# Kernel optimization log

Measured on AMD Instinct MI355X. Metric: run time of the kernel, lower is better.

## Reference

```python
import jax, jax.numpy as jnp
import numpy as np

N = 50000      # nodes
E = 800000     # edges (avg degree 16)
DIM = 256      # in_channels == heads * out_channels
H = 8          # heads
C = DIM // H   # per-head out_channels = 32
EDGE_DIM = 2
NEG_SLOPE = 0.2


def setup_inputs() -> dict:
    key = jax.random.key(0)
    ks = jax.random.split(key, 8)
    x = jax.random.normal(ks[0], (N, DIM), dtype=jnp.float32)
    edge_index = jax.random.randint(ks[1], (2, E), 0, N, dtype=jnp.int32)
    edge_attr = jax.random.normal(ks[2], (E, EDGE_DIM), dtype=jnp.float32)
    s = 1.0 / np.sqrt(DIM)
    W_l = jax.random.normal(ks[3], (DIM, H * C), dtype=jnp.float32) * s   # lin_l (src)
    W_r = jax.random.normal(ks[4], (DIM, H * C), dtype=jnp.float32) * s   # lin_r (dst)
    W_e = jax.random.normal(ks[5], (EDGE_DIM, H * C), dtype=jnp.float32) * (1.0 / np.sqrt(EDGE_DIM))
    att = jax.random.normal(ks[6], (H, C), dtype=jnp.float32) * s         # attention vector a
    bias = jnp.zeros((H * C,), dtype=jnp.float32)
    return {"x": x, "edge_index": edge_index, "edge_attr": edge_attr,
            "W_l": W_l, "W_r": W_r, "W_e": W_e, "att": att, "bias": bias}


def reference(x, edge_index, edge_attr, W_l, W_r, W_e, att, bias):
    src, dst = edge_index[0], edge_index[1]
    # --- add self loops; fill_value='mean' => scatter-mean of incoming edge_attr per node ---
    attr_sum = jax.ops.segment_sum(edge_attr, dst, num_segments=N)          # [N, 2]
    cnt = jax.ops.segment_sum(jnp.ones((edge_attr.shape[0], 1), edge_attr.dtype), dst, num_segments=N)
    loop_attr = attr_sum / jnp.maximum(cnt, 1.0)                             # [N, 2], 0 for isolated nodes
    idx = jnp.arange(N, dtype=src.dtype)
    src_a = jnp.concatenate([src, idx])                                      # [E+N]
    dst_a = jnp.concatenate([dst, idx])
    ea = jnp.concatenate([edge_attr, loop_attr], axis=0)                     # [E+N, 2]
    # --- GATv2: project src/dst/edge features ---
    x_l = (x @ W_l).reshape(N, H, C)
    x_r = (x @ W_r).reshape(N, H, C)
    e_e = (ea @ W_e).reshape(-1, H, C)                                       # [E+N, H, C]
    m = x_l[src_a] + x_r[dst_a] + e_e                                        # [E+N, H, C]
    score = jnp.einsum('ehc,hc->eh', jax.nn.leaky_relu(m, NEG_SLOPE), att)   # [E+N, H]
    # --- segment softmax over incoming edges of each dst (self loop guarantees >=1 edge) ---
    smax = jax.ops.segment_max(score, dst_a, num_segments=N)                 # [N, H]
    ex = jnp.exp(score - smax[dst_a])
    denom = jax.ops.segment_sum(ex, dst_a, num_segments=N)                   # [N, H]
    alpha = ex / denom[dst_a]                                                # [E+N, H]
    # --- weighted scatter-add of src messages ---
    out = jax.ops.segment_sum(alpha[..., None] * x_l[src_a], dst_a, num_segments=N)  # [N, H, C]
    return out.reshape(N, H * C) + bias
```

## Files before the change

### kernel.cpp

```cpp
#include <hip/hip_runtime.h>
#include <hip/hip_bf16.h>

#define NN 50000
#define EE 800000
#define DIM 256
#define ROWC 64
#define NEG_SLOPE 0.2f
#define LOG2E 1.44269504088896f

#define GEMM_BLOCKS 1564
#define CF_BLOCKS   3125
#define ZERO_BLOCKS 49
#define WT_BLOCKS   512

typedef __attribute__((ext_vector_type(8))) short short8;
typedef __attribute__((ext_vector_type(4))) float f32x4;
typedef __attribute__((ext_vector_type(2))) float v2f;

__device__ __forceinline__ unsigned short f2bf(float f) {
    unsigned u = __float_as_uint(f);
    unsigned r = (u + 0x7fffu + ((u >> 16) & 1u)) >> 16;
    return (unsigned short)r;
}
__device__ __forceinline__ float u2f_lo(unsigned u) {
    return __uint_as_float(u << 16);
}
__device__ __forceinline__ float u2f_hi(unsigned u) {
    return __uint_as_float(u & 0xffff0000u);
}

__device__ __forceinline__ float red8(float s) {
    int t;
    t = __builtin_amdgcn_update_dpp(0, __float_as_int(s), 0xB1, 0xF, 0xF, true);
    s += __int_as_float(t);
    t = __builtin_amdgcn_update_dpp(0, __float_as_int(s), 0x4E, 0xF, 0xF, true);
    s += __int_as_float(t);
    t = __builtin_amdgcn_update_dpp(0, __float_as_int(s), 0x141, 0xF, 0xF, true);
    s += __int_as_float(t);
    return s;
}

__global__ __launch_bounds__(256) void k_prep0(
    const float* __restrict__ Wl, const float* __restrict__ Wr,
    unsigned short* __restrict__ wt, int* __restrict__ cnt)
{
    int b = blockIdx.x;
    if (b < ZERO_BLOCKS) {
        *(int4*)(cnt + (b * 256 + threadIdx.x) * 4) = make_int4(0, 0, 0, 0);
    } else {
        int idx = (b - ZERO_BLOCKS) * 256 + threadIdx.x;
        int n = idx >> 8, k = idx & 255;
        float v = (n < 256) ? Wl[k * 256 + n] : Wr[k * 256 + (n - 256)];
        wt[idx] = f2bf(v);
    }
}

__global__ __launch_bounds__(256) void k_main(
    const float* __restrict__ x, const unsigned short* __restrict__ wt,
    const int* __restrict__ ei, const float* __restrict__ ea,
    int* __restrict__ cnt, unsigned short* __restrict__ xl,
    unsigned short* __restrict__ xr, uint2* __restrict__ edge_rec)
{
    __shared__ short sAB[12288];
    int tid = threadIdx.x;

    if (blockIdx.x >= GEMM_BLOCKS) {
        int e = (blockIdx.x - GEMM_BLOCKS) * 256 + tid;
        int src = ei[e];
        int dst = ei[EE + e];
        float2 a = *(const float2*)(ea + 2 * e);
        int rl = atomicAdd(cnt + dst, 1);
        if (rl < ROWC) {
            unsigned packed = ((unsigned)f2bf(a.y) << 16) | f2bf(a.x);
            edge_rec[(size_t)dst * ROWC + rl] = make_uint2((unsigned)src, packed);
        }
        return;
    }

    int bid = blockIdx.x;
    const int q = GEMM_BLOCKS / 8, r = GEMM_BLOCKS % 8;
    int xcd = bid & 7, kk = bid >> 3;
    int wg = (xcd < r) ? xcd * (q + 1) + kk
                       : r * (q + 1) + (xcd - r) * q + kk;

    int wid = tid >> 6, lane = tid & 63;
    int mt = wg >> 2, nt = wg & 3;
    int mBase = mt * 128, nBase = nt * 128;
    int wm = (wid & 1) * 64, wn = (wid >> 1) * 64;
    int qq4 = lane >> 4, mh = lane & 15;

    f32x4 acc[4][4];
#pragma unroll
    for (int i = 0; i < 4; ++i)
#pragma unroll
        for (int j = 0; j < 4; ++j)
            acc[i][j] = (f32x4){0.f, 0.f, 0.f, 0.f};

    int aoffF[4], boff[4];
#pragma unroll
    for (int f = 0; f < 4; ++f) {
        int rr = wm + f * 16 + mh;
        aoffF[f] = rr * 32 + ((qq4 ^ (rr & 3)) << 3);
        int nl = wn + f * 16 + mh;
        boff[f] = 8192 + (nl * 4 + (qq4 ^ (nl & 3))) * 8;
    }

    for (int k0 = 0; k0 < 256; k0 += 32) {
        __syncthreads();
#pragma unroll
        for (int it = 0; it < 6; ++it) {
            int L = it * 256 + tid;
            const void* g;
            if (L < 1024) {
                int rr = L >> 3;
                int qs = (L >> 1) & 3, hf = L & 1;
                int q2 = qs ^ (rr & 3);
                int grow = mBase + rr;
                if (grow > NN - 1) grow = NN - 1;
                g = (const void*)(x + (size_t)grow * 256 + k0 + q2 * 8 + hf * 4);
            } else {
                int LB = L - 1024;
                int nl = LB >> 2;
                int q2 = (LB & 3) ^ (nl & 3);
                g = (const void*)(wt + (size_t)(nBase + nl) * 256 + k0 + q2 * 8);
            }
            short* lp = sAB + (it * 256 + wid * 64) * 8;
            __builtin_amdgcn_global_load_lds(
                (const __attribute__((address_space(1))) void*)g,
                (__attribute__((address_space(3))) void*)lp, 16, 0, 0);
        }
        __syncthreads();

        short8 af[4], bfr[4];
        const float* sAf = (const float*)sAB;
#pragma unroll
        for (int f = 0; f < 4; ++f) {
            f32x4 lo = *(const f32x4*)(sAf + aoffF[f]);
            f32x4 hi = *(const f32x4*)(sAf + aoffF[f] + 4);
            uint4 up;
            asm("v_cvt_pk_bf16_f32 %0, %1, %2" : "=v"(up.x) : "v"(lo[0]), "v"(lo[1]));
            asm("v_cvt_pk_bf16_f32 %0, %1, %2" : "=v"(up.y) : "v"(lo[2]), "v"(lo[3]));
            asm("v_cvt_pk_bf16_f32 %0, %1, %2" : "=v"(up.z) : "v"(hi[0]), "v"(hi[1]));
            asm("v_cvt_pk_bf16_f32 %0, %1, %2" : "=v"(up.w) : "v"(hi[2]), "v"(hi[3]));
            af[f] = *(short8*)&up;
        }
#pragma unroll
        for (int f = 0; f < 4; ++f) bfr[f] = *(const short8*)(sAB + boff[f]);
#pragma unroll
        for (int i = 0; i < 4; ++i)
#pragma unroll
            for (int j = 0; j < 4; ++j)
                acc[i][j] = __builtin_amdgcn_mfma_f32_16x16x32_bf16(
                    af[i], bfr[j], acc[i][j], 0, 0, 0);
    }

    unsigned short* cb = (nt < 2) ? xl : xr;
    int chalf = (nt & 1) * 128;
#pragma unroll
    for (int i = 0; i < 4; ++i)
#pragma unroll
        for (int j = 0; j < 4; ++j)
#pragma unroll
            for (int rr = 0; rr < 4; ++rr) {
                int row = mBase + wm + i * 16 + qq4 * 4 + rr;
                if (row < NN) {
                    int col = chalf + wn + j * 16 + mh;
                    cb[(size_t)row * 256 + col] = f2bf(acc[i][j][rr]);
                }
            }
}

__global__ __launch_bounds__(256) void k_attn(
    const unsigned short* __restrict__ xl, const unsigned short* __restrict__ xr,
    const int* __restrict__ cnt, const uint2* __restrict__ edge_rec,
    const float* __restrict__ W_e, const float* __restrict__ att,
    const float* __restrict__ bias, float* __restrict__ out)
{
    int n = __builtin_amdgcn_readfirstlane(blockIdx.x * 4 + (threadIdx.x >> 6));
    if (n >= NN) return;
    int lane = threadIdx.x & 63;
    int j = lane * 4;

    uint2 xru = *(const uint2*)(xr + ((size_t)n << 8) + j);
    v2f xr01 = {u2f_lo(xru.x), u2f_hi(xru.x)};
    v2f xr23 = {u2f_lo(xru.y), u2f_hi(xru.y)};
    float4 av = *(const float4*)(att + j);
    v2f att01 = {av.x * LOG2E, av.y * LOG2E};
    v2f att23 = {av.z * LOG2E, av.w * LOG2E};
    float4 w0v = *(const float4*)(W_e + j);
    float4 w1v = *(const float4*)(W_e + 256 + j);
    v2f we0_01 = {w0v.x, w0v.y}, we0_23 = {w0v.z, w0v.w};
    v2f we1_01 = {w1v.x, w1v.y}, we1_23 = {w1v.z, w1v.w};
    const v2f sl2 = {NEG_SLOPE, NEG_SLOPE};

    int cn = __builtin_amdgcn_readfirstlane(cnt[n]);
    if (cn > ROWC) cn = ROWC;
    int rs = n << 6;

    float D = 0.0f, la0 = 0.0f, la1 = 0.0f;
    v2f acc01 = {0.f, 0.f}, acc23 = {0.f, 0.f};

    auto body = [&](uint2 ru, float a0, float a1) {
        v2f xl01 = {u2f_lo(ru.x), u2f_hi(ru.x)};
        v2f xl23 = {u2f_lo(ru.y), u2f_hi(ru.y)};
        v2f a0v = {a0, a0}, a1v = {a1, a1};
        v2f m01 = xl01 + xr01;
        v2f m23 = xl23 + xr23;
        m01 = __builtin_elementwise_fma(a0v, we0_01, m01);
        m23 = __builtin_elementwise_fma(a0v, we0_23, m23);
        m01 = __builtin_elementwise_fma(a1v, we1_01, m01);
        m23 = __builtin_elementwise_fma(a1v, we1_23, m23);
        v2f t01 = __builtin_elementwise_max(m01, m01 * sl2);
        v2f t23 = __builtin_elementwise_max(m23, m23 * sl2);
        v2f sv = t01 * att01;
        sv = __builtin_elementwise_fma(t23, att23, sv);
        float s = sv.x + sv.y;
        s = red8(s);
        float w = __builtin_amdgcn_exp2f(s);
        D += w;
        v2f wv = {w, w};
        acc01 = __builtin_elementwise_fma(wv, xl01, acc01);
        acc23 = __builtin_elementwise_fma(wv, xl23, acc23);
    };

    if (cn > 0) {
        uint2 rc = edge_rec[rs + lane];
        int rcx = (int)rc.x, rca = (int)rc.y;

        auto gat = [&](int k) -> uint2 {
            unsigned sidx = (unsigned)__builtin_amdgcn_readlane(rcx, k);
            if (sidx > NN - 1) sidx = 0;
            return *(const uint2*)(xl + ((size_t)sidx << 8) + j);
        };
        auto proc = [&](uint2 xu, int k) {
            unsigned pk = (unsigned)__builtin_amdgcn_readlane(rca, k);
            float a0 = __uint_as_float(pk << 16);
            float a1 = __uint_as_float(pk & 0xffff0000u);
            la0 += a0; la1 += a1;
            body(xu, a0, a1);
        };

        int m = cn;
        uint2 x0 = gat(0), x1 = gat(1), x2 = gat(2), x3 = gat(3);
        uint2 x4 = gat(4), x5 = gat(5), x6 = gat(6), x7 = gat(7);
        for (int i = 0; i < m; i += 8) {
            proc(x0, i);
            if (i +  8 < m) x0 = gat(i +  8);
            if (i + 1 < m) { proc(x1, i + 1); if (i +  9 < m) x1 = gat(i +  9); }
            if (i + 2 < m) { proc(x2, i + 2); if (i + 10 < m) x2 = gat(i + 10); }
            if (i + 3 < m) { proc(x3, i + 3); if (i + 11 < m) x3 = gat(i + 11); }
            if (i + 4 < m) { proc(x4, i + 4); if (i + 12 < m) x4 = gat(i + 12); }
            if (i + 5 < m) { proc(x5, i + 5); if (i + 13 < m) x5 = gat(i + 13); }
            if (i + 6 < m) { proc(x6, i + 6); if (i + 14 < m) x6 = gat(i + 14); }
            if (i + 7 < m) { proc(x7, i + 7); if (i + 15 < m) x7 = gat(i + 15); }
        }
    }

    float invc = 1.0f / fmaxf((float)cn, 1.0f);
    uint2 xs = *(const uint2*)(xl + ((size_t)n << 8) + j);
    body(xs, la0 * invc, la1 * invc);

    float invD = 1.0f / D;
    float4 b4 = *(const float4*)(bias + j);
    float4 o;
    o.x = fmaf(acc01.x, invD, b4.x);
    o.y = fmaf(acc01.y, invD, b4.y);
    o.z = fmaf(acc23.x, invD, b4.z);
    o.w = fmaf(acc23.y, invD, b4.w);
    *(float4*)(out + (size_t)n * 256 + j) = o;
}

extern "C" void kernel_launch(void* const* d_in, const int* in_sizes, int n_in,
                              void* d_out, int out_size, void* d_ws, size_t ws_size,
                              hipStream_t stream)
{
    const float* x    = (const float*)d_in[0];
    const int*   ei   = (const int*)  d_in[1];
    const float* ea   = (const float*)d_in[2];
    const float* Wl   = (const float*)d_in[3];
    const float* Wr   = (const float*)d_in[4];
    const float* We   = (const float*)d_in[5];
    const float* att  = (const float*)d_in[6];
    const float* bias = (const float*)d_in[7];
    float* out = (float*)d_out;

    char* ws = (char*)d_ws;
    size_t off = 0;
    unsigned short* xl = (unsigned short*)(ws + off); off += (size_t)NN * 256 * 2;
    unsigned short* xr = (unsigned short*)(ws + off); off += (size_t)NN * 256 * 2;
    uint2*  edge_rec   = (uint2*)(ws + off);          off += (size_t)(NN * ROWC + 128) * 8;
    int*    cnt        = (int*)(ws + off);            off += (size_t)(ZERO_BLOCKS * 1024) * 4;
    unsigned short* wt = (unsigned short*)(ws + off); off += (size_t)512 * 256 * 2;

    k_prep0 <<<ZERO_BLOCKS + WT_BLOCKS, 256, 0, stream>>>(Wl, Wr, wt, cnt);
    k_main  <<<GEMM_BLOCKS + CF_BLOCKS, 256, 0, stream>>>(
        x, wt, ei, ea, cnt, xl, xr, edge_rec);
    k_attn  <<<12500, 256, 0, stream>>>(
        xl, xr, cnt, edge_rec, We, att, bias, out);
}
```

Measured before the change: 242.8 us.

## Split edge bucketing by destination range and overlap with attention kernels

Edge bucketing is split into three destination-node ranges. The first runs alongside the GEMM and the next two run inside the attention launches for node ranges already fully bucketed. The attention work is split across three kernels so each range's scatter overlaps with compute on earlier ranges. In exchange, the destination indices are re-read three times and an extra kernel launch is added.

```diff
diff --git a/kernel.cpp b/kernel.cpp
--- a/kernel.cpp
+++ b/kernel.cpp
@@ -8,10 +8,16 @@
 #define NEG_SLOPE 0.2f
 #define LOG2E 1.44269504088896f
 
+#define D1 16668
+#define D2 33336
+
+#define CF_BLOCKS   3125
 #define GEMM_BLOCKS 1564
-#define CF_BLOCKS   3125
 #define ZERO_BLOCKS 49
 #define WT_BLOCKS   512
+#define ATTN_A_BLOCKS 4167
+#define ATTN_B_BLOCKS 4167
+#define ATTN_C_BLOCKS 4166
 
 typedef __attribute__((ext_vector_type(8))) short short8;
 typedef __attribute__((ext_vector_type(4))) float f32x4;
@@ -40,6 +46,122 @@
     return s;
 }
 
+__device__ __forceinline__ void cf_range(
+    const int* __restrict__ ei, const float* __restrict__ ea,
+    int* __restrict__ cnt, uint2* __restrict__ edge_rec,
+    int blk, int tid, int dlo, int dhi)
+{
+    int e = blk * 256 + tid;
+    int dst = ei[EE + e];
+    if (dst >= dlo && dst < dhi) {
+        int src = ei[e];
+        float2 a = *(const float2*)(ea + 2 * e);
+        int rl = atomicAdd(cnt + dst, 1);
+        if (rl < ROWC) {
+            unsigned packed = ((unsigned)f2bf(a.y) << 16) | f2bf(a.x);
+            edge_rec[(size_t)dst * ROWC + rl] = make_uint2((unsigned)src, packed);
+        }
+    }
+}
+
+__device__ __forceinline__ void attn_node(
+    const unsigned short* __restrict__ xl, const unsigned short* __restrict__ xr,
+    const int* __restrict__ cnt, const uint2* __restrict__ edge_rec,
+    const float* __restrict__ W_e, const float* __restrict__ att,
+    const float* __restrict__ bias, float* __restrict__ out,
+    int n, int lane)
+{
+    int j = lane * 4;
+
+    uint2 xru = *(const uint2*)(xr + ((size_t)n << 8) + j);
+    v2f xr01 = {u2f_lo(xru.x), u2f_hi(xru.x)};
+    v2f xr23 = {u2f_lo(xru.y), u2f_hi(xru.y)};
+    float4 av = *(const float4*)(att + j);
+    v2f att01 = {av.x * LOG2E, av.y * LOG2E};
+    v2f att23 = {av.z * LOG2E, av.w * LOG2E};
+    float4 w0v = *(const float4*)(W_e + j);
+    float4 w1v = *(const float4*)(W_e + 256 + j);
+    v2f we0_01 = {w0v.x, w0v.y}, we0_23 = {w0v.z, w0v.w};
+    v2f we1_01 = {w1v.x, w1v.y}, we1_23 = {w1v.z, w1v.w};
+    const v2f sl2 = {NEG_SLOPE, NEG_SLOPE};
+
+    int cn = __builtin_amdgcn_readfirstlane(cnt[n]);
+    if (cn > ROWC) cn = ROWC;
+    int rs = n << 6;
+
+    float D = 0.0f, la0 = 0.0f, la1 = 0.0f;
+    v2f acc01 = {0.f, 0.f}, acc23 = {0.f, 0.f};
+
+    auto body = [&](uint2 ru, float a0, float a1) {
+        v2f xl01 = {u2f_lo(ru.x), u2f_hi(ru.x)};
+        v2f xl23 = {u2f_lo(ru.y), u2f_hi(ru.y)};
+        v2f a0v = {a0, a0}, a1v = {a1, a1};
+        v2f m01 = xl01 + xr01;
+        v2f m23 = xl23 + xr23;
+        m01 = __builtin_elementwise_fma(a0v, we0_01, m01);
+        m23 = __builtin_elementwise_fma(a0v, we0_23, m23);
+        m01 = __builtin_elementwise_fma(a1v, we1_01, m01);
+        m23 = __builtin_elementwise_fma(a1v, we1_23, m23);
+        v2f t01 = __builtin_elementwise_max(m01, m01 * sl2);
+        v2f t23 = __builtin_elementwise_max(m23, m23 * sl2);
+        v2f sv = t01 * att01;
+        sv = __builtin_elementwise_fma(t23, att23, sv);
+        float s = sv.x + sv.y;
+        s = red8(s);
+        float w = __builtin_amdgcn_exp2f(s);
+        D += w;
+        v2f wv = {w, w};
+        acc01 = __builtin_elementwise_fma(wv, xl01, acc01);
+        acc23 = __builtin_elementwise_fma(wv, xl23, acc23);
+    };
+
+    if (cn > 0) {
+        uint2 rc = edge_rec[rs + lane];
+        int rcx = (int)rc.x, rca = (int)rc.y;
+
+        auto gat = [&](int k) -> uint2 {
+            unsigned sidx = (unsigned)__builtin_amdgcn_readlane(rcx, k);
+            if (sidx > NN - 1) sidx = 0;
+            return *(const uint2*)(xl + ((size_t)sidx << 8) + j);
+        };
+        auto proc = [&](uint2 xu, int k) {
+            unsigned pk = (unsigned)__builtin_amdgcn_readlane(rca, k);
+            float a0 = __uint_as_float(pk << 16);
+            float a1 = __uint_as_float(pk & 0xffff0000u);
+            la0 += a0; la1 += a1;
+            body(xu, a0, a1);
+        };
+
+        int m = cn;
+        uint2 x0 = gat(0), x1 = gat(1), x2 = gat(2), x3 = gat(3);
+        uint2 x4 = gat(4), x5 = gat(5), x6 = gat(6), x7 = gat(7);
+        for (int i = 0; i < m; i += 8) {
+            proc(x0, i);
+            if (i +  8 < m) x0 = gat(i +  8);
+            if (i + 1 < m) { proc(x1, i + 1); if (i +  9 < m) x1 = gat(i +  9); }
+            if (i + 2 < m) { proc(x2, i + 2); if (i + 10 < m) x2 = gat(i + 10); }
+            if (i + 3 < m) { proc(x3, i + 3); if (i + 11 < m) x3 = gat(i + 11); }
+            if (i + 4 < m) { proc(x4, i + 4); if (i + 12 < m) x4 = gat(i + 12); }
+            if (i + 5 < m) { proc(x5, i + 5); if (i + 13 < m) x5 = gat(i + 13); }
+            if (i + 6 < m) { proc(x6, i + 6); if (i + 14 < m) x6 = gat(i + 14); }
+            if (i + 7 < m) { proc(x7, i + 7); if (i + 15 < m) x7 = gat(i + 15); }
+        }
+    }
+
+    float invc = 1.0f / fmaxf((float)cn, 1.0f);
+    uint2 xs = *(const uint2*)(xl + ((size_t)n << 8) + j);
+    body(xs, la0 * invc, la1 * invc);
+
+    float invD = 1.0f / D;
+    float4 b4 = *(const float4*)(bias + j);
+    float4 o;
+    o.x = fmaf(acc01.x, invD, b4.x);
+    o.y = fmaf(acc01.y, invD, b4.y);
+    o.z = fmaf(acc23.x, invD, b4.z);
+    o.w = fmaf(acc23.y, invD, b4.w);
+    *(float4*)(out + (size_t)n * 256 + j) = o;
+}
+
 __global__ __launch_bounds__(256) void k_prep0(
     const float* __restrict__ Wl, const float* __restrict__ Wr,
     unsigned short* __restrict__ wt, int* __restrict__ cnt)
@@ -55,7 +177,7 @@
     }
 }
 
-__global__ __launch_bounds__(256) void k_main(
+__global__ __launch_bounds__(256) void k_mainA(
     const float* __restrict__ x, const unsigned short* __restrict__ wt,
     const int* __restrict__ ei, const float* __restrict__ ea,
     int* __restrict__ cnt, unsigned short* __restrict__ xl,
@@ -64,20 +186,12 @@
     __shared__ short sAB[12288];
     int tid = threadIdx.x;
 
-    if (blockIdx.x >= GEMM_BLOCKS) {
-        int e = (blockIdx.x - GEMM_BLOCKS) * 256 + tid;
-        int src = ei[e];
-        int dst = ei[EE + e];
-        float2 a = *(const float2*)(ea + 2 * e);
-        int rl = atomicAdd(cnt + dst, 1);
-        if (rl < ROWC) {
-            unsigned packed = ((unsigned)f2bf(a.y) << 16) | f2bf(a.x);
-            edge_rec[(size_t)dst * ROWC + rl] = make_uint2((unsigned)src, packed);
-        }
+    if (blockIdx.x < CF_BLOCKS) {
+        cf_range(ei, ea, cnt, edge_rec, blockIdx.x, tid, 0, D1);
         return;
     }
 
-    int bid = blockIdx.x;
+    int bid = blockIdx.x - CF_BLOCKS;
     const int q = GEMM_BLOCKS / 8, r = GEMM_BLOCKS % 8;
     int xcd = bid & 7, kk = bid >> 3;
     int wg = (xcd < r) ? xcd * (q + 1) + kk
@@ -170,104 +284,50 @@
             }
 }
 
-__global__ __launch_bounds__(256) void k_attn(
+__global__ __launch_bounds__(256) void k_phase2(
+    const int* __restrict__ ei, const float* __restrict__ ea,
+    int* __restrict__ cnt, uint2* __restrict__ edge_rec,
+    const unsigned short* __restrict__ xl, const unsigned short* __restrict__ xr,
+    const float* __restrict__ W_e, const float* __restrict__ att,
+    const float* __restrict__ bias, float* __restrict__ out)
+{
+    int tid = threadIdx.x;
+    if (blockIdx.x < CF_BLOCKS) {
+        cf_range(ei, ea, cnt, edge_rec, blockIdx.x, tid, D1, D2);
+        return;
+    }
+    int n = __builtin_amdgcn_readfirstlane(
+        (blockIdx.x - CF_BLOCKS) * 4 + (tid >> 6));
+    attn_node(xl, xr, cnt, edge_rec, W_e, att, bias, out, n, tid & 63);
+}
+
+__global__ __launch_bounds__(256) void k_phase3(
+    const int* __restrict__ ei, const float* __restrict__ ea,
+    int* __restrict__ cnt, uint2* __restrict__ edge_rec,
+    const unsigned short* __restrict__ xl, const unsigned short* __restrict__ xr,
+    const float* __restrict__ W_e, const float* __restrict__ att,
+    const float* __restrict__ bias, float* __restrict__ out)
+{
+    int tid = threadIdx.x;
+    if (blockIdx.x < CF_BLOCKS) {
+        cf_range(ei, ea, cnt, edge_rec, blockIdx.x, tid, D2, NN);
+        return;
+    }
+    int n = __builtin_amdgcn_readfirstlane(
+        D1 + (blockIdx.x - CF_BLOCKS) * 4 + (tid >> 6));
+    attn_node(xl, xr, cnt, edge_rec, W_e, att, bias, out, n, tid & 63);
+}
+
+__global__ __launch_bounds__(256) void k_attnC(
     const unsigned short* __restrict__ xl, const unsigned short* __restrict__ xr,
     const int* __restrict__ cnt, const uint2* __restrict__ edge_rec,
     const float* __restrict__ W_e, const float* __restrict__ att,
     const float* __restrict__ bias, float* __restrict__ out)
 {
-    int n = __builtin_amdgcn_readfirstlane(blockIdx.x * 4 + (threadIdx.x >> 6));
+    int n = __builtin_amdgcn_readfirstlane(
+        D2 + blockIdx.x * 4 + (threadIdx.x >> 6));
     if (n >= NN) return;
-    int lane = threadIdx.x & 63;
-    int j = lane * 4;
-
-    uint2 xru = *(const uint2*)(xr + ((size_t)n << 8) + j);
-    v2f xr01 = {u2f_lo(xru.x), u2f_hi(xru.x)};
-    v2f xr23 = {u2f_lo(xru.y), u2f_hi(xru.y)};
-    float4 av = *(const float4*)(att + j);
-    v2f att01 = {av.x * LOG2E, av.y * LOG2E};
-    v2f att23 = {av.z * LOG2E, av.w * LOG2E};
-    float4 w0v = *(const float4*)(W_e + j);
-    float4 w1v = *(const float4*)(W_e + 256 + j);
-    v2f we0_01 = {w0v.x, w0v.y}, we0_23 = {w0v.z, w0v.w};
-    v2f we1_01 = {w1v.x, w1v.y}, we1_23 = {w1v.z, w1v.w};
-    const v2f sl2 = {NEG_SLOPE, NEG_SLOPE};
-
-    int cn = __builtin_amdgcn_readfirstlane(cnt[n]);
-    if (cn > ROWC) cn = ROWC;
-    int rs = n << 6;
-
-    float D = 0.0f, la0 = 0.0f, la1 = 0.0f;
-    v2f acc01 = {0.f, 0.f}, acc23 = {0.f, 0.f};
-
-    auto body = [&](uint2 ru, float a0, float a1) {
-        v2f xl01 = {u2f_lo(ru.x), u2f_hi(ru.x)};
-        v2f xl23 = {u2f_lo(ru.y), u2f_hi(ru.y)};
-        v2f a0v = {a0, a0}, a1v = {a1, a1};
-        v2f m01 = xl01 + xr01;
-        v2f m23 = xl23 + xr23;
-        m01 = __builtin_elementwise_fma(a0v, we0_01, m01);
-        m23 = __builtin_elementwise_fma(a0v, we0_23, m23);
-        m01 = __builtin_elementwise_fma(a1v, we1_01, m01);
-        m23 = __builtin_elementwise_fma(a1v, we1_23, m23);
-        v2f t01 = __builtin_elementwise_max(m01, m01 * sl2);
-        v2f t23 = __builtin_elementwise_max(m23, m23 * sl2);
-        v2f sv = t01 * att01;
-        sv = __builtin_elementwise_fma(t23, att23, sv);
-        float s = sv.x + sv.y;
-        s = red8(s);
-        float w = __builtin_amdgcn_exp2f(s);
-        D += w;
-        v2f wv = {w, w};
-        acc01 = __builtin_elementwise_fma(wv, xl01, acc01);
-        acc23 = __builtin_elementwise_fma(wv, xl23, acc23);
-    };
-
-    if (cn > 0) {
-        uint2 rc = edge_rec[rs + lane];
-        int rcx = (int)rc.x, rca = (int)rc.y;
-
-        auto gat = [&](int k) -> uint2 {
-            unsigned sidx = (unsigned)__builtin_amdgcn_readlane(rcx, k);
-            if (sidx > NN - 1) sidx = 0;
-            return *(const uint2*)(xl + ((size_t)sidx << 8) + j);
-        };
-        auto proc = [&](uint2 xu, int k) {
-            unsigned pk = (unsigned)__builtin_amdgcn_readlane(rca, k);
-            float a0 = __uint_as_float(pk << 16);
-            float a1 = __uint_as_float(pk & 0xffff0000u);
-            la0 += a0; la1 += a1;
-            body(xu, a0, a1);
-        };
-
-        int m = cn;
-        uint2 x0 = gat(0), x1 = gat(1), x2 = gat(2), x3 = gat(3);
-        uint2 x4 = gat(4), x5 = gat(5), x6 = gat(6), x7 = gat(7);
-        for (int i = 0; i < m; i += 8) {
-            proc(x0, i);
-            if (i +  8 < m) x0 = gat(i +  8);
-            if (i + 1 < m) { proc(x1, i + 1); if (i +  9 < m) x1 = gat(i +  9); }
-            if (i + 2 < m) { proc(x2, i + 2); if (i + 10 < m) x2 = gat(i + 10); }
-            if (i + 3 < m) { proc(x3, i + 3); if (i + 11 < m) x3 = gat(i + 11); }
-            if (i + 4 < m) { proc(x4, i + 4); if (i + 12 < m) x4 = gat(i + 12); }
-            if (i + 5 < m) { proc(x5, i + 5); if (i + 13 < m) x5 = gat(i + 13); }
-            if (i + 6 < m) { proc(x6, i + 6); if (i + 14 < m) x6 = gat(i + 14); }
-            if (i + 7 < m) { proc(x7, i + 7); if (i + 15 < m) x7 = gat(i + 15); }
-        }
-    }
-
-    float invc = 1.0f / fmaxf((float)cn, 1.0f);
-    uint2 xs = *(const uint2*)(xl + ((size_t)n << 8) + j);
-    body(xs, la0 * invc, la1 * invc);
-
-    float invD = 1.0f / D;
-    float4 b4 = *(const float4*)(bias + j);
-    float4 o;
-    o.x = fmaf(acc01.x, invD, b4.x);
-    o.y = fmaf(acc01.y, invD, b4.y);
-    o.z = fmaf(acc23.x, invD, b4.z);
-    o.w = fmaf(acc23.y, invD, b4.w);
-    *(float4*)(out + (size_t)n * 256 + j) = o;
+    attn_node(xl, xr, cnt, edge_rec, W_e, att, bias, out, n, threadIdx.x & 63);
 }
 
 extern "C" void kernel_launch(void* const* d_in, const int* in_sizes, int n_in,
@@ -293,8 +353,12 @@
     unsigned short* wt = (unsigned short*)(ws + off); off += (size_t)512 * 256 * 2;
 
     k_prep0 <<<ZERO_BLOCKS + WT_BLOCKS, 256, 0, stream>>>(Wl, Wr, wt, cnt);
-    k_main  <<<GEMM_BLOCKS + CF_BLOCKS, 256, 0, stream>>>(
+    k_mainA <<<CF_BLOCKS + GEMM_BLOCKS, 256, 0, stream>>>(
         x, wt, ei, ea, cnt, xl, xr, edge_rec);
-    k_attn  <<<12500, 256, 0, stream>>>(
+    k_phase2<<<CF_BLOCKS + ATTN_A_BLOCKS, 256, 0, stream>>>(
+        ei, ea, cnt, edge_rec, xl, xr, We, att, bias, out);
+    k_phase3<<<CF_BLOCKS + ATTN_B_BLOCKS, 256, 0, stream>>>(
+        ei, ea, cnt, edge_rec, xl, xr, We, att, bias, out);
+    k_attnC <<<ATTN_C_BLOCKS, 256, 0, stream>>>(
         xl, xr, cnt, edge_rec, We, att, bias, out);
 }
```

Measured after the change: 276.7 us. 14.0% more time.

## Replace global atomic edge bucketing with LDS histogram plus column prefix-scan fill

Applied to the files above, without the earlier changes.

Replaces per-edge global atomicAdd on a count array with a two-pass scheme. Each of 128 blocks first builds a 16-bit packed LDS histogram of destination nodes over its edge chunk. A column pass then computes each block's exclusive offsets and per-node degree alongside the GEMM. A separate fill kernel re-counts in LDS to place edge records deterministically. This removes contended global atomics, but adds an extra kernel launch, a 12.8 MB histogram buffer that must be written and read, and a fill pass with only 128 blocks that may underuse the GPU.

```diff
diff --git a/kernel.cpp b/kernel.cpp
--- a/kernel.cpp
+++ b/kernel.cpp
@@ -8,10 +8,13 @@
 #define NEG_SLOPE 0.2f
 #define LOG2E 1.44269504088896f
 
+#define CSTR 50000
+#define HIST_BLOCKS 128
+#define EPB 6250
+#define HIST_ITERS 13
+#define WT_BLOCKS 256
+#define COLS_BLOCKS 196
 #define GEMM_BLOCKS 1564
-#define CF_BLOCKS   3125
-#define ZERO_BLOCKS 49
-#define WT_BLOCKS   512
 
 typedef __attribute__((ext_vector_type(8))) short short8;
 typedef __attribute__((ext_vector_type(4))) float f32x4;
@@ -40,39 +43,56 @@
     return s;
 }
 
-__global__ __launch_bounds__(256) void k_prep0(
+__global__ __launch_bounds__(512) void k_prep_hist(
     const float* __restrict__ Wl, const float* __restrict__ Wr,
-    unsigned short* __restrict__ wt, int* __restrict__ cnt)
-{
-    int b = blockIdx.x;
-    if (b < ZERO_BLOCKS) {
-        *(int4*)(cnt + (b * 256 + threadIdx.x) * 4) = make_int4(0, 0, 0, 0);
+    const int* __restrict__ ei,
+    unsigned short* __restrict__ wt, unsigned short* __restrict__ ghist)
+{
+    __shared__ unsigned lh[CSTR / 2];
+    int b = blockIdx.x, tid = threadIdx.x;
+    if (b < HIST_BLOCKS) {
+        for (int i = tid; i < CSTR / 2; i += 512) lh[i] = 0u;
+        __syncthreads();
+        int base = b * EPB;
+#pragma unroll
+        for (int it = 0; it < HIST_ITERS; ++it) {
+            int idx = it * 512 + tid;
+            if (idx < EPB) {
+                int dst = ei[EE + base + idx];
+                atomicAdd(&lh[dst >> 1], 1u << ((dst & 1) * 16));
+            }
+        }
+        __syncthreads();
+        unsigned* gout = (unsigned*)(ghist + (size_t)b * CSTR);
+        for (int i = tid; i < CSTR / 2; i += 512) gout[i] = lh[i];
     } else {
-        int idx = (b - ZERO_BLOCKS) * 256 + threadIdx.x;
+        int idx = (b - HIST_BLOCKS) * 512 + tid;
         int n = idx >> 8, k = idx & 255;
         float v = (n < 256) ? Wl[k * 256 + n] : Wr[k * 256 + (n - 256)];
         wt[idx] = f2bf(v);
     }
 }
 
-__global__ __launch_bounds__(256) void k_main(
+__global__ __launch_bounds__(256) void k_gemmcol(
     const float* __restrict__ x, const unsigned short* __restrict__ wt,
-    const int* __restrict__ ei, const float* __restrict__ ea,
-    int* __restrict__ cnt, unsigned short* __restrict__ xl,
-    unsigned short* __restrict__ xr, uint2* __restrict__ edge_rec)
+    unsigned short* __restrict__ ghist, int* __restrict__ deg,
+    unsigned short* __restrict__ xl, unsigned short* __restrict__ xr)
 {
     __shared__ short sAB[12288];
     int tid = threadIdx.x;
 
     if (blockIdx.x >= GEMM_BLOCKS) {
-        int e = (blockIdx.x - GEMM_BLOCKS) * 256 + tid;
-        int src = ei[e];
-        int dst = ei[EE + e];
-        float2 a = *(const float2*)(ea + 2 * e);
-        int rl = atomicAdd(cnt + dst, 1);
-        if (rl < ROWC) {
-            unsigned packed = ((unsigned)f2bf(a.y) << 16) | f2bf(a.x);
-            edge_rec[(size_t)dst * ROWC + rl] = make_uint2((unsigned)src, packed);
+        int d = (blockIdx.x - GEMM_BLOCKS) * 256 + tid;
+        if (d < CSTR) {
+            unsigned s = 0;
+#pragma unroll 8
+            for (int b = 0; b < HIST_BLOCKS; ++b) {
+                size_t o = (size_t)b * CSTR + d;
+                unsigned v = ghist[o];
+                ghist[o] = (unsigned short)s;
+                s += v;
+            }
+            deg[d] = (int)s;
         }
         return;
     }
@@ -170,9 +190,39 @@
             }
 }
 
+__global__ __launch_bounds__(512) void k_fill(
+    const int* __restrict__ ei, const float* __restrict__ ea,
+    const unsigned short* __restrict__ ghist, uint2* __restrict__ edge_rec)
+{
+    __shared__ unsigned lh[CSTR / 2];
+    int tid = threadIdx.x, blk = blockIdx.x;
+    for (int i = tid; i < CSTR / 2; i += 512) lh[i] = 0u;
+    __syncthreads();
+    int base = blk * EPB;
+    const unsigned short* gh = ghist + (size_t)blk * CSTR;
+#pragma unroll
+    for (int it = 0; it < HIST_ITERS; ++it) {
+        int idx = it * 512 + tid;
+        if (idx < EPB) {
+            int e = base + idx;
+            int src = ei[e];
+            int dst = ei[EE + e];
+            float2 a = *(const float2*)(ea + 2 * e);
+            unsigned sh = (dst & 1) * 16;
+            unsigned old = atomicAdd(&lh[dst >> 1], 1u << sh);
+            int wr = (int)gh[dst] + (int)((old >> sh) & 0xffffu);
+            if (wr < ROWC) {
+                unsigned packed = ((unsigned)f2bf(a.y) << 16) | f2bf(a.x);
+                edge_rec[(size_t)dst * ROWC + wr] =
+                    make_uint2((unsigned)src, packed);
+            }
+        }
+    }
+}
+
 __global__ __launch_bounds__(256) void k_attn(
     const unsigned short* __restrict__ xl, const unsigned short* __restrict__ xr,
-    const int* __restrict__ cnt, const uint2* __restrict__ edge_rec,
+    const int* __restrict__ deg, const uint2* __restrict__ edge_rec,
     const float* __restrict__ W_e, const float* __restrict__ att,
     const float* __restrict__ bias, float* __restrict__ out)
 {
@@ -193,7 +243,7 @@
     v2f we1_01 = {w1v.x, w1v.y}, we1_23 = {w1v.z, w1v.w};
     const v2f sl2 = {NEG_SLOPE, NEG_SLOPE};
 
-    int cn = __builtin_amdgcn_readfirstlane(cnt[n]);
+    int cn = __builtin_amdgcn_readfirstlane(deg[n]);
     if (cn > ROWC) cn = ROWC;
     int rs = n << 6;
 
@@ -288,13 +338,15 @@
     size_t off = 0;
     unsigned short* xl = (unsigned short*)(ws + off); off += (size_t)NN * 256 * 2;
     unsigned short* xr = (unsigned short*)(ws + off); off += (size_t)NN * 256 * 2;
-    uint2*  edge_rec   = (uint2*)(ws + off);          off += (size_t)(NN * ROWC + 128) * 8;
-    int*    cnt        = (int*)(ws + off);            off += (size_t)(ZERO_BLOCKS * 1024) * 4;
+    uint2*  edge_rec   = (uint2*)(ws + off);          off += (size_t)NN * ROWC * 8;
+    unsigned short* ghist = (unsigned short*)(ws + off); off += (size_t)HIST_BLOCKS * CSTR * 2;
+    int*    deg        = (int*)(ws + off);            off += (size_t)NN * 4;
     unsigned short* wt = (unsigned short*)(ws + off); off += (size_t)512 * 256 * 2;
 
-    k_prep0 <<<ZERO_BLOCKS + WT_BLOCKS, 256, 0, stream>>>(Wl, Wr, wt, cnt);
-    k_main  <<<GEMM_BLOCKS + CF_BLOCKS, 256, 0, stream>>>(
-        x, wt, ei, ea, cnt, xl, xr, edge_rec);
-    k_attn  <<<12500, 256, 0, stream>>>(
-        xl, xr, cnt, edge_rec, We, att, bias, out);
-}
+    k_prep_hist<<<HIST_BLOCKS + WT_BLOCKS, 512, 0, stream>>>(Wl, Wr, ei, wt, ghist);
+    k_gemmcol  <<<GEMM_BLOCKS + COLS_BLOCKS, 256, 0, stream>>>(
+        x, wt, ghist, deg, xl, xr);
+    k_fill     <<<HIST_BLOCKS, 512, 0, stream>>>(ei, ea, ghist, edge_rec);
+    k_attn     <<<12500, 256, 0, stream>>>(
+        xl, xr, deg, edge_rec, We, att, bias, out);
+}
```

After: 270.3 us. 1.11x slower.

## Process two destination nodes per wavefront with 8-wide bf16 lanes in attention

Applied to the files above, without the earlier changes.

The attention kernel now assigns two destination nodes to each 64-lane wavefront, one per 32-lane half, and each lane handles 8 channels with 16-byte gathers instead of 4 channels with 8-byte gathers. The per-head score reduction shrinks from three DPP steps to two, and the grid is halved. Each half loops to the larger of the two nodes' edge counts and masks out invalid edges, so the work in a wave is set by the busier node. Edge records are read in 32-entry chunks to fit this layout. The aim is wider memory transactions and fewer waves for the gather-bound aggregation, at the cost of more registers per lane.

```diff
diff --git a/kernel.cpp b/kernel.cpp
--- a/kernel.cpp
+++ b/kernel.cpp
@@ -8,8 +8,8 @@
 #define NEG_SLOPE 0.2f
 #define LOG2E 1.44269504088896f
 
+#define CF_BLOCKS   3125
 #define GEMM_BLOCKS 1564
-#define CF_BLOCKS   3125
 #define ZERO_BLOCKS 49
 #define WT_BLOCKS   512
 
@@ -29,13 +29,11 @@
     return __uint_as_float(u & 0xffff0000u);
 }
 
-__device__ __forceinline__ float red8(float s) {
+__device__ __forceinline__ float red4(float s) {
     int t;
     t = __builtin_amdgcn_update_dpp(0, __float_as_int(s), 0xB1, 0xF, 0xF, true);
     s += __int_as_float(t);
     t = __builtin_amdgcn_update_dpp(0, __float_as_int(s), 0x4E, 0xF, 0xF, true);
-    s += __int_as_float(t);
-    t = __builtin_amdgcn_update_dpp(0, __float_as_int(s), 0x141, 0xF, 0xF, true);
     s += __int_as_float(t);
     return s;
 }
@@ -176,98 +174,140 @@
     const float* __restrict__ W_e, const float* __restrict__ att,
     const float* __restrict__ bias, float* __restrict__ out)
 {
-    int n = __builtin_amdgcn_readfirstlane(blockIdx.x * 4 + (threadIdx.x >> 6));
-    if (n >= NN) return;
-    int lane = threadIdx.x & 63;
-    int j = lane * 4;
-
-    uint2 xru = *(const uint2*)(xr + ((size_t)n << 8) + j);
+    int tid = threadIdx.x;
+    int lane = tid & 63;
+    int h = lane >> 5;
+    int lane32 = lane & 31;
+    int n = blockIdx.x * 8 + ((tid >> 6) << 1) + h;
+    int j = lane32 * 8;
+
+    uint4 xru = *(const uint4*)(xr + ((size_t)n << 8) + j);
     v2f xr01 = {u2f_lo(xru.x), u2f_hi(xru.x)};
     v2f xr23 = {u2f_lo(xru.y), u2f_hi(xru.y)};
-    float4 av = *(const float4*)(att + j);
-    v2f att01 = {av.x * LOG2E, av.y * LOG2E};
-    v2f att23 = {av.z * LOG2E, av.w * LOG2E};
-    float4 w0v = *(const float4*)(W_e + j);
-    float4 w1v = *(const float4*)(W_e + 256 + j);
-    v2f we0_01 = {w0v.x, w0v.y}, we0_23 = {w0v.z, w0v.w};
-    v2f we1_01 = {w1v.x, w1v.y}, we1_23 = {w1v.z, w1v.w};
+    v2f xr45 = {u2f_lo(xru.z), u2f_hi(xru.z)};
+    v2f xr67 = {u2f_lo(xru.w), u2f_hi(xru.w)};
+    float4 aL = *(const float4*)(att + j);
+    float4 aH = *(const float4*)(att + j + 4);
+    v2f att01 = {aL.x * LOG2E, aL.y * LOG2E};
+    v2f att23 = {aL.z * LOG2E, aL.w * LOG2E};
+    v2f att45 = {aH.x * LOG2E, aH.y * LOG2E};
+    v2f att67 = {aH.z * LOG2E, aH.w * LOG2E};
+    float4 w0L = *(const float4*)(W_e + j);
+    float4 w0H = *(const float4*)(W_e + j + 4);
+    float4 w1L = *(const float4*)(W_e + 256 + j);
+    float4 w1H = *(const float4*)(W_e + 256 + j + 4);
+    v2f we0_01 = {w0L.x, w0L.y}, we0_23 = {w0L.z, w0L.w};
+    v2f we0_45 = {w0H.x, w0H.y}, we0_67 = {w0H.z, w0H.w};
+    v2f we1_01 = {w1L.x, w1L.y}, we1_23 = {w1L.z, w1L.w};
+    v2f we1_45 = {w1H.x, w1H.y}, we1_67 = {w1H.z, w1H.w};
     const v2f sl2 = {NEG_SLOPE, NEG_SLOPE};
 
-    int cn = __builtin_amdgcn_readfirstlane(cnt[n]);
-    if (cn > ROWC) cn = ROWC;
-    int rs = n << 6;
+    int cnv = cnt[n];
+    if (cnv > ROWC) cnv = ROWC;
+    int cnA = __builtin_amdgcn_readlane(cnv, 0);
+    int cnB = __builtin_amdgcn_readlane(cnv, 32);
+    int mmax = cnA > cnB ? cnA : cnB;
 
     float D = 0.0f, la0 = 0.0f, la1 = 0.0f;
     v2f acc01 = {0.f, 0.f}, acc23 = {0.f, 0.f};
-
-    auto body = [&](uint2 ru, float a0, float a1) {
+    v2f acc45 = {0.f, 0.f}, acc67 = {0.f, 0.f};
+
+    auto body = [&](uint4 ru, float a0, float a1, bool valid) {
         v2f xl01 = {u2f_lo(ru.x), u2f_hi(ru.x)};
         v2f xl23 = {u2f_lo(ru.y), u2f_hi(ru.y)};
+        v2f xl45 = {u2f_lo(ru.z), u2f_hi(ru.z)};
+        v2f xl67 = {u2f_lo(ru.w), u2f_hi(ru.w)};
         v2f a0v = {a0, a0}, a1v = {a1, a1};
-        v2f m01 = xl01 + xr01;
-        v2f m23 = xl23 + xr23;
+        v2f m01 = xl01 + xr01, m23 = xl23 + xr23;
+        v2f m45 = xl45 + xr45, m67 = xl67 + xr67;
         m01 = __builtin_elementwise_fma(a0v, we0_01, m01);
         m23 = __builtin_elementwise_fma(a0v, we0_23, m23);
+        m45 = __builtin_elementwise_fma(a0v, we0_45, m45);
+        m67 = __builtin_elementwise_fma(a0v, we0_67, m67);
         m01 = __builtin_elementwise_fma(a1v, we1_01, m01);
         m23 = __builtin_elementwise_fma(a1v, we1_23, m23);
+        m45 = __builtin_elementwise_fma(a1v, we1_45, m45);
+        m67 = __builtin_elementwise_fma(a1v, we1_67, m67);
         v2f t01 = __builtin_elementwise_max(m01, m01 * sl2);
         v2f t23 = __builtin_elementwise_max(m23, m23 * sl2);
+        v2f t45 = __builtin_elementwise_max(m45, m45 * sl2);
+        v2f t67 = __builtin_elementwise_max(m67, m67 * sl2);
         v2f sv = t01 * att01;
         sv = __builtin_elementwise_fma(t23, att23, sv);
+        sv = __builtin_elementwise_fma(t45, att45, sv);
+        sv = __builtin_elementwise_fma(t67, att67, sv);
         float s = sv.x + sv.y;
-        s = red8(s);
+        s = red4(s);
         float w = __builtin_amdgcn_exp2f(s);
+        w = valid ? w : 0.0f;
         D += w;
         v2f wv = {w, w};
         acc01 = __builtin_elementwise_fma(wv, xl01, acc01);
         acc23 = __builtin_elementwise_fma(wv, xl23, acc23);
+        acc45 = __builtin_elementwise_fma(wv, xl45, acc45);
+        acc67 = __builtin_elementwise_fma(wv, xl67, acc67);
+        la0 += a0; la1 += a1;
     };
 
-    if (cn > 0) {
-        uint2 rc = edge_rec[rs + lane];
+    for (int cb = 0; cb < ROWC; cb += 32) {
+        int rem = mmax - cb;
+        if (rem <= 0) break;
+        int mm = rem > 32 ? 32 : rem;
+        uint2 rc = edge_rec[((size_t)n << 6) + cb + lane32];
         int rcx = (int)rc.x, rca = (int)rc.y;
 
-        auto gat = [&](int k) -> uint2 {
-            unsigned sidx = (unsigned)__builtin_amdgcn_readlane(rcx, k);
+        auto gat = [&](int k) -> uint4 {
+            int sA = __builtin_amdgcn_readlane(rcx, k);
+            int sB = __builtin_amdgcn_readlane(rcx, 32 + k);
+            unsigned sidx = (unsigned)(h ? sB : sA);
             if (sidx > NN - 1) sidx = 0;
-            return *(const uint2*)(xl + ((size_t)sidx << 8) + j);
+            return *(const uint4*)(xl + ((size_t)sidx << 8) + j);
         };
-        auto proc = [&](uint2 xu, int k) {
-            unsigned pk = (unsigned)__builtin_amdgcn_readlane(rca, k);
+        auto proc = [&](uint4 xu, int k) {
+            int pA = __builtin_amdgcn_readlane(rca, k);
+            int pB = __builtin_amdgcn_readlane(rca, 32 + k);
+            unsigned pk = (unsigned)(h ? pB : pA);
+            bool valid = (cb + k) < cnv;
+            if (!valid) pk = 0u;
             float a0 = __uint_as_float(pk << 16);
             float a1 = __uint_as_float(pk & 0xffff0000u);
-            la0 += a0; la1 += a1;
-            body(xu, a0, a1);
+            body(xu, a0, a1, valid);
         };
 
-        int m = cn;
-        uint2 x0 = gat(0), x1 = gat(1), x2 = gat(2), x3 = gat(3);
-        uint2 x4 = gat(4), x5 = gat(5), x6 = gat(6), x7 = gat(7);
-        for (int i = 0; i < m; i += 8) {
+        uint4 x0 = gat(0), x1 = gat(1), x2 = gat(2), x3 = gat(3);
+        uint4 x4 = gat(4), x5 = gat(5), x6 = gat(6), x7 = gat(7);
+        for (int i = 0; i < mm; i += 8) {
             proc(x0, i);
-            if (i +  8 < m) x0 = gat(i +  8);
-            if (i + 1 < m) { proc(x1, i + 1); if (i +  9 < m) x1 = gat(i +  9); }
-            if (i + 2 < m) { proc(x2, i + 2); if (i + 10 < m) x2 = gat(i + 10); }
-            if (i + 3 < m) { proc(x3, i + 3); if (i + 11 < m) x3 = gat(i + 11); }
-            if (i + 4 < m) { proc(x4, i + 4); if (i + 12 < m) x4 = gat(i + 12); }
-            if (i + 5 < m) { proc(x5, i + 5); if (i + 13 < m) x5 = gat(i + 13); }
-            if (i + 6 < m) { proc(x6, i + 6); if (i + 14 < m) x6 = gat(i + 14); }
-            if (i + 7 < m) { proc(x7, i + 7); if (i + 15 < m) x7 = gat(i + 15); }
+            if (i +  8 < mm) x0 = gat(i +  8);
+            if (i + 1 < mm) { proc(x1, i + 1); if (i +  9 < mm) x1 = gat(i +  9); }
+            if (i + 2 < mm) { proc(x2, i + 2); if (i + 10 < mm) x2 = gat(i + 10); }
+            if (i + 3 < mm) { proc(x3, i + 3); if (i + 11 < mm) x3 = gat(i + 11); }
+            if (i + 4 < mm) { proc(x4, i + 4); if (i + 12 < mm) x4 = gat(i + 12); }
+            if (i + 5 < mm) { proc(x5, i + 5); if (i + 13 < mm) x5 = gat(i + 13); }
+            if (i + 6 < mm) { proc(x6, i + 6); if (i + 14 < mm) x6 = gat(i + 14); }
+            if (i + 7 < mm) { proc(x7, i + 7); if (i + 15 < mm) x7 = gat(i + 15); }
         }
     }
 
-    float invc = 1.0f / fmaxf((float)cn, 1.0f);
-    uint2 xs = *(const uint2*)(xl + ((size_t)n << 8) + j);
-    body(xs, la0 * invc, la1 * invc);
+    float invc = 1.0f / fmaxf((float)cnv, 1.0f);
+    uint4 xs = *(const uint4*)(xl + ((size_t)n << 8) + j);
+    body(xs, la0 * invc, la1 * invc, true);
 
     float invD = 1.0f / D;
-    float4 b4 = *(const float4*)(bias + j);
-    float4 o;
-    o.x = fmaf(acc01.x, invD, b4.x);
-    o.y = fmaf(acc01.y, invD, b4.y);
-    o.z = fmaf(acc23.x, invD, b4.z);
-    o.w = fmaf(acc23.y, invD, b4.w);
-    *(float4*)(out + (size_t)n * 256 + j) = o;
+    float4 bL = *(const float4*)(bias + j);
+    float4 bH = *(const float4*)(bias + j + 4);
+    float4 o0, o1;
+    o0.x = fmaf(acc01.x, invD, bL.x);
+    o0.y = fmaf(acc01.y, invD, bL.y);
+    o0.z = fmaf(acc23.x, invD, bL.z);
+    o0.w = fmaf(acc23.y, invD, bL.w);
+    o1.x = fmaf(acc45.x, invD, bH.x);
+    o1.y = fmaf(acc45.y, invD, bH.y);
+    o1.z = fmaf(acc67.x, invD, bH.z);
+    o1.w = fmaf(acc67.y, invD, bH.w);
+    float* op = out + (size_t)n * 256 + j;
+    *(float4*)(op) = o0;
+    *(float4*)(op + 4) = o1;
 }
 
 extern "C" void kernel_launch(void* const* d_in, const int* in_sizes, int n_in,
@@ -295,6 +335,6 @@
     k_prep0 <<<ZERO_BLOCKS + WT_BLOCKS, 256, 0, stream>>>(Wl, Wr, wt, cnt);
     k_main  <<<GEMM_BLOCKS + CF_BLOCKS, 256, 0, stream>>>(
         x, wt, ei, ea, cnt, xl, xr, edge_rec);
-    k_attn  <<<12500, 256, 0, stream>>>(
+    k_attn  <<<6250, 256, 0, stream>>>(
         xl, xr, cnt, edge_rec, We, att, bias, out);
 }
```

Result: slower. 249.3 us (+2.7%).
